# Kernel tuning notes

Measured on AMD Instinct MI355X. Metric: run time of the kernel, lower is better.

The kernel has to match this reference:

```python
import jax, jax.numpy as jnp
import numpy as np

# OAdder2d_Q, mode='oconv', in_bit=16, w_bit=16 (dorefa), bias=False, no augment.
# Physical model (O2NN-style differential detection):
#   y = sum_{c,i,j} [ x*w*sin(phi)*(d0+d1)/2 + (x^2 + w^2)*(d0-d1)/4 ]
# With ideal disks (d0=d1=1) the square terms vanish and the op reduces to a
# conv whose effective kernel is w * sin(phi); default oconv phases are -pi/2
# for the first C//2 input channels and +pi/2 for the rest.

IN_BIT = 16
W_BIT = 16
STRIDE = 1
PADDING = 1
B, C, O, K, H, W = 32, 128, 256, 3, 56, 56


def _ste_round(v, n):
    # straight-through round (forward value == torch uniform_quantize)
    return v + jax.lax.stop_gradient(jnp.round(v * n) / n - v)


def input_quantize(x):
    n = float(2 ** IN_BIT - 1)
    return _ste_round(jnp.clip(x, 0.0, 1.0), n)


def weight_quantize(w):
    # dorefa, w_bit > 1
    n = float(2 ** W_BIT - 1)
    t = jnp.tanh(w)
    t = t / (2.0 * jnp.max(jnp.abs(t))) + 0.5
    return _ste_round(t, n)


def _conv(x, k):
    return jax.lax.conv_general_dilated(
        x, k, (STRIDE, STRIDE), [(PADDING, PADDING), (PADDING, PADDING)],
        dimension_numbers=("NCHW", "OIHW", "NCHW"))


def optical_conv2d(x_q, w_q, phases, disks):
    s = jnp.sin(phases)[0, 0]                  # (C,k,k)
    d0 = disks[0, 0, ..., 0]                   # (C,k,k)
    d1 = disks[0, 0, ..., 1]
    k_mul = w_q * (s * (d0 + d1) * 0.5)        # effective conv kernel (O,C,k,k)
    y = _conv(x_q, k_mul)                      # (N,O,H,W)
    coef = (d0 - d1) * 0.25                    # zero for ideal disks
    y_sq = _conv(x_q * x_q, coef[None])        # (N,1,H,W), broadcasts over O
    w_term = jnp.sum(w_q * w_q * coef[None], axis=(1, 2, 3))  # (O,)
    return y + y_sq + w_term[None, :, None, None]


def setup_inputs() -> dict:
    key = jax.random.key(0)
    k1, k2 = jax.random.split(key)
    x = jax.random.uniform(k1, (B, C, H, W), dtype=jnp.float32)
    fan_in = C * K * K
    weight = jax.random.normal(k2, (O, C, K, K), dtype=jnp.float32) * np.sqrt(2.0 / fan_in)
    phases = jnp.concatenate([
        jnp.full((1, 1, C // 2, K, K), -np.pi / 2, dtype=jnp.float32),
        jnp.full((1, 1, C - C // 2, K, K), np.pi / 2, dtype=jnp.float32)], axis=2)
    disks = jnp.ones((1, 1, C, K, K, 2), dtype=jnp.float32)
    return {"x": x, "weight": weight, "phases": phases, "disks": disks}


def reference(x, weight, phases, disks):
    x_q = input_quantize(x)
    w_q = weight_quantize(weight)
    return optical_conv2d(x_q, w_q, phases, disks)
```

## Files before the change

### kernel.cpp

```cpp
#include <hip/hip_runtime.h>
#include <math.h>

typedef __attribute__((ext_vector_type(8))) short short8;
typedef __attribute__((ext_vector_type(4))) float floatx4;

#define BB 32
#define CC 128
#define OO 256
#define HH 56
#define WW 56
#define HWSZ 3136
#define NPIX 100352
#define WELEM 294912
#define QN 65535.0f
#define QINV (1.0f/65535.0f)

#define MAXB_OFF   0
#define CFLAG_OFF  128
#define WTERM_OFF  256
#define COEF_OFF   2048
#define KEFF_OFF   8192
#define YSQ_OFF    598016
#define XQP_OFF    1048576
#define XQP_BYTES  30408704ull
#define WS_NEED    (XQP_OFF + XQP_BYTES)
#define KEFF32_OFF 8192

__device__ __forceinline__ float quant_x(float v) {
    v = fminf(fmaxf(v, 0.0f), 1.0f);
    return rintf(v * QN) * QINV;
}

__device__ __forceinline__ unsigned short f2bf(float f) {
    unsigned u = __float_as_uint(f);
    u += 0x7fffu + ((u >> 16) & 1u);
    return (unsigned short)(u >> 16);
}

__device__ __forceinline__ void gl16(const void* g, void* l) {
    __builtin_amdgcn_global_load_lds(
        (const __attribute__((address_space(1))) unsigned char*)g,
        (__attribute__((address_space(3))) unsigned char*)l, 16, 0, 0);
}

__global__ void kmax_kernel(const float* __restrict__ w, unsigned* __restrict__ maxout) {
    int i = blockIdx.x * blockDim.x + threadIdx.x;
    float m = 0.0f;
    for (int idx = i; idx < WELEM; idx += gridDim.x * blockDim.x)
        m = fmaxf(m, fabsf(w[idx]));
    #pragma unroll
    for (int off = 32; off; off >>= 1)
        m = fmaxf(m, __shfl_down(m, off));
    __shared__ float red[4];
    if ((threadIdx.x & 63) == 0) red[threadIdx.x >> 6] = m;
    __syncthreads();
    if (threadIdx.x == 0) {
        m = fmaxf(fmaxf(red[0], red[1]), fmaxf(red[2], red[3]));
        atomicMax(maxout, __float_as_uint(m));
    }
}

__global__ void kprep_kernel(const float* __restrict__ wt, const float* __restrict__ phases,
                             const float* __restrict__ disks, const unsigned* __restrict__ maxbits,
                             unsigned short* __restrict__ kefft, float* __restrict__ coef,
                             unsigned* __restrict__ cflag, float* __restrict__ wterm) {
    int idx = blockIdx.x * blockDim.x + threadIdx.x;
    if (idx >= WELEM) return;
    int kk = idx % 9;
    int c  = (idx / 9) % CC;
    int o  = idx / (9 * CC);
    float M = tanhf(__uint_as_float(*maxbits));
    float t = tanhf(wt[idx]);
    float v = t / (2.0f * M) + 0.5f;
    float wq = rintf(v * QN) * QINV;
    int pidx = c * 9 + kk;
    float s  = sinf(phases[pidx]);
    float d0 = disks[pidx * 2 + 0];
    float d1 = disks[pidx * 2 + 1];
    float kv = wq * (s * (d0 + d1) * 0.5f);

    int step = kk * 4 + (c >> 5);
    int ot = o >> 7, lo = o & 127;
    int wm = lo >> 6, mf = (lo >> 4) & 3, l15 = lo & 15;
    int kg = (c >> 3) & 3, e = c & 7;
    size_t byte = (size_t)(step * 2 + ot) * 8192
                + wm * 4096 + mf * 1024 + (kg * 16 + l15) * 16 + e * 2;
    kefft[byte >> 1] = f2bf(kv);

    float cf = (d0 - d1) * 0.25f;
    if (o == 0) {
        coef[kk * CC + c] = cf;
        if (cf != 0.0f) atomicOr(cflag, 1u);
    }
    float contrib = wq * wq * cf;
    if (contrib != 0.0f) atomicAdd(wterm + o, contrib);
}

__global__ __launch_bounds__(256) void kborder_kernel(unsigned short* __restrict__ xqp) {
    int t = threadIdx.x;
    int id = blockIdx.x * 256 + t;
    int b = blockIdx.y;
    int pxi = id >> 4, chunk = id & 15;
    int h, w;
    if (pxi < 128) { h = (pxi >> 6) * 57; w = pxi & 63; }
    else { int r = pxi - 128; h = 1 + (r >> 3); int wi = r & 7; w = wi == 0 ? 0 : 56 + wi; }
    short8 z = (short8)0;
    *reinterpret_cast<short8*>((char*)xqp + (size_t)b * 3801088ull
                               + ((size_t)(h * 64 + w)) * 256 + chunk * 16) = z;
}

__global__ __launch_bounds__(256) void kxqpad_kernel(const float* __restrict__ x,
                                                     unsigned short* __restrict__ xqp) {
    __shared__ __align__(16) unsigned short tile[64][136];
    int t = threadIdx.x;
    int b = blockIdx.y;
    int hw0 = blockIdx.x * 64;
    const float* xb = x + (size_t)b * (CC * HWSZ) + hw0;
    #pragma unroll
    for (int rep = 0; rep < 32; ++rep) {
        int lin = rep * 256 + t;
        int c = lin >> 6, j = lin & 63;
        float v = xb[(size_t)c * HWSZ + j];
        tile[j][c] = f2bf(quant_x(v));
    }
    __syncthreads();
    unsigned short* xq_b = xqp + (size_t)b * (58 * 64 * 128);
    #pragma unroll
    for (int rep = 0; rep < 4; ++rep) {
        int lin = rep * 256 + t;
        int c16 = lin & 15, j = lin >> 4;
        int hw = hw0 + j;
        int h = hw / WW, w = hw - h * WW;
        short8 v = *reinterpret_cast<const short8*>(&tile[j][c16 * 8]);
        *reinterpret_cast<short8*>(xq_b + ((size_t)((h + 1) * 64 + (w + 1))) * 128 + c16 * 8) = v;
    }
}

__global__ __launch_bounds__(256) void ysq_kernel(const float* __restrict__ x,
                                                  const float* __restrict__ coef,
                                                  const unsigned* __restrict__ cflag,
                                                  float* __restrict__ ysq) {
    int t = threadIdx.x;
    int P = blockIdx.x * 256 + t;
    if (*cflag == 0u) {
        ysq[P] = 0.0f;
        return;
    }
    __shared__ float cf[9 * CC];
    for (int i = t; i < 9 * CC; i += 256) cf[i] = coef[i];
    __syncthreads();
    int b = P / HWSZ; int hw = P - b * HWSZ;
    int h = hw / WW;  int w = hw - h * WW;
    const float* xb = x + (size_t)b * (CC * HWSZ);
    float s2 = 0.0f;
    #pragma unroll
    for (int kk = 0; kk < 9; ++kk) {
        int dh = kk / 3 - 1, dw = kk % 3 - 1;
        int ih = h + dh, iw = w + dw;
        bool valid = ((unsigned)ih < HH) && ((unsigned)iw < WW);
        int ihc = min(max(ih, 0), HH - 1), iwc = min(max(iw, 0), WW - 1);
        const float* xp = xb + ihc * WW + iwc;
        float fm = valid ? 1.0f : 0.0f;
        const float* cp = cf + kk * CC;
        #pragma unroll 4
        for (int c = 0; c < CC; ++c) {
            float xv = quant_x(xp[(size_t)c * HWSZ]) * fm;
            s2 = fmaf(xv * xv, cp[c], s2);
        }
    }
    ysq[P] = s2;
}

__global__ __launch_bounds__(256, 2) void oconv_kernel(
        const unsigned short* __restrict__ xqp,
        const unsigned short* __restrict__ keff,
        const float* __restrict__ ysq,
        const float* __restrict__ wterm,
        float* __restrict__ out) {
    __shared__ __align__(16) char smem[32768];
    const int t  = threadIdx.x;
    const int id  = blockIdx.x;
    const int swz = (id & 7) * 196 + (id >> 3);
    const int bx  = swz >> 1;
    const int oty = swz & 1;

    const char* xb = (const char*)xqp;
    long bb0, bb1;
    {
        int pxA  = ((t >> 6) << 4) + (t & 15);
        int cOff = ((t >> 4) & 3) * 16;
        int P0 = bx * 128 + pxA;
        int b0 = P0 / HWSZ, hw0 = P0 - b0 * HWSZ;
        int h0 = hw0 / WW,  w0 = hw0 - h0 * WW;
        bb0 = ((long)((b0 * 58 + h0 + 1) * 64 + (w0 + 1))) * 256 + cOff;
        int P1 = P0 + 64;
        int b1 = P1 / HWSZ, hw1 = P1 - b1 * HWSZ;
        int h1 = hw1 / WW,  w1 = hw1 - h1 * WW;
        bb1 = ((long)((b1 * 58 + h1 + 1) * 64 + (w1 + 1))) * 256 + cOff;
    }

    const int l15 = t & 15;
    const int kg  = (t >> 4) & 3;
    const int wid = t >> 6;
    const int wm  = wid >> 1, wn = wid & 1;
    const int lane16 = (t & 63) * 16;

    floatx4 acc[4][4];
    #pragma unroll
    for (int i = 0; i < 4; ++i)
        #pragma unroll
        for (int j = 0; j < 4; ++j) acc[i][j] = (floatx4)0.0f;

    auto stage = [&](int buf, int s) {
        char* la = smem + buf * 16384 + t * 16;
        const char* ga = (const char*)keff + (size_t)(s * 2 + oty) * 8192 + t * 16;
        gl16(ga,        la);
        gl16(ga + 4096, la + 4096);
        int kk = s >> 2, cs = s & 3;
        int dh = kk / 3, dw = kk - dh * 3;
        long bo = (long)((dh - 1) * 64 + (dw - 1)) * 256 + cs * 64;
        char* lb = la + 8192;
        gl16(xb + bb0 + bo, lb);
        gl16(xb + bb1 + bo, lb + 4096);
    };

    auto compute = [&](int buf) {
        const char* base = smem + buf * 16384;
        const char* ap = base + wm * 4096 + lane16;
        const char* bp = base + 8192 + wn * 4096 + lane16;
        short8 a[4], b[4];
        #pragma unroll
        for (int mf = 0; mf < 4; ++mf)
            a[mf] = *reinterpret_cast<const short8*>(ap + mf * 1024);
        #pragma unroll
        for (int nf = 0; nf < 4; ++nf)
            b[nf] = *reinterpret_cast<const short8*>(bp + nf * 1024);
        #pragma unroll
        for (int mf = 0; mf < 4; ++mf)
            #pragma unroll
            for (int nf = 0; nf < 4; ++nf)
                acc[mf][nf] = __builtin_amdgcn_mfma_f32_16x16x32_bf16(a[mf], b[nf], acc[mf][nf], 0, 0, 0);
    };

    stage(0, 0);
    stage(1, 1);
    for (int s = 0; s < 36; ++s) {
        if (s < 35) { asm volatile("s_waitcnt vmcnt(4)" ::: "memory"); }
        else        { asm volatile("s_waitcnt vmcnt(0)" ::: "memory"); }
        __builtin_amdgcn_sched_barrier(0);
        __builtin_amdgcn_s_barrier();
        compute(s & 1);
        asm volatile("s_waitcnt lgkmcnt(0)" ::: "memory");
        __builtin_amdgcn_sched_barrier(0);
        __builtin_amdgcn_s_barrier();
        if (s < 34) stage(s & 1, s + 2);
    }

    float wv[4][4];
    #pragma unroll
    for (int mf = 0; mf < 4; ++mf)
        #pragma unroll
        for (int j = 0; j < 4; ++j)
            wv[mf][j] = wterm[oty * 128 + wm * 64 + mf * 16 + kg * 4 + j];

    #pragma unroll
    for (int nf = 0; nf < 4; ++nf) {
        int P = bx * 128 + wn * 64 + nf * 16 + l15;
        int b = P / HWSZ; int hw = P - b * HWSZ;
        float yv = ysq[P];
        float* op = out + (size_t)b * (OO * HWSZ) + hw;
        #pragma unroll
        for (int mf = 0; mf < 4; ++mf)
            #pragma unroll
            for (int j = 0; j < 4; ++j) {
                int o = oty * 128 + wm * 64 + mf * 16 + kg * 4 + j;
                op[(size_t)o * HWSZ] = acc[mf][nf][j] + yv + wv[mf][j];
            }
    }
}

__global__ void kprep32_kernel(const float* __restrict__ wt, const float* __restrict__ phases,
                               const float* __restrict__ disks, const unsigned* __restrict__ maxbits,
                               float* __restrict__ keff, float* __restrict__ coef,
                               float* __restrict__ wterm) {
    int idx = blockIdx.x * blockDim.x + threadIdx.x;
    if (idx >= WELEM) return;
    int kk = idx % 9;
    int c  = (idx / 9) % CC;
    int o  = idx / (9 * CC);
    float M = tanhf(__uint_as_float(*maxbits));
    float t = tanhf(wt[idx]);
    float v = t / (2.0f * M) + 0.5f;
    float wq = rintf(v * QN) * QINV;
    int pidx = c * 9 + kk;
    float s  = sinf(phases[pidx]);
    float d0 = disks[pidx * 2 + 0];
    float d1 = disks[pidx * 2 + 1];
    keff[(kk * CC + c) * OO + o] = wq * (s * (d0 + d1) * 0.5f);
    float cf = (d0 - d1) * 0.25f;
    if (o == 0) coef[kk * CC + c] = cf;
    float contrib = wq * wq * cf;
    if (contrib != 0.0f) atomicAdd(wterm + o, contrib);
}

__global__ __launch_bounds__(256) void kconv32_kernel(
        const float* __restrict__ xsrc, const float* __restrict__ keff,
        const float* __restrict__ coef, const float* __restrict__ wterm,
        float* __restrict__ out) {
    int t   = blockIdx.x * 256 + threadIdx.x;
    int ocb = blockIdx.y * 16;
    int b   = t / HWSZ;
    int rem = t - b * HWSZ;
    int h   = rem / WW;
    int w   = rem - h * WW;
    float acc[16];
    #pragma unroll
    for (int i = 0; i < 16; ++i) acc[i] = 0.0f;
    float s2 = 0.0f;
    const float* xb = xsrc + (size_t)b * (CC * HWSZ);
    #pragma unroll
    for (int kh = 0; kh < 3; ++kh) {
        #pragma unroll
        for (int kw = 0; kw < 3; ++kw) {
            int ih = h + kh - 1, iw = w + kw - 1;
            bool valid = ((unsigned)ih < HH) && ((unsigned)iw < WW);
            int ihc = min(max(ih, 0), HH - 1);
            int iwc = min(max(iw, 0), WW - 1);
            const float* xp   = xb + ihc * WW + iwc;
            const float* wrow = keff + (kh * 3 + kw) * (CC * OO) + ocb;
            const float* cfp  = coef + (kh * 3 + kw) * CC;
            float fm = valid ? 1.0f : 0.0f;
            #pragma unroll 4
            for (int c = 0; c < CC; ++c) {
                float xv = quant_x(xp[c * HWSZ]) * fm;
                s2 = fmaf(xv * xv, cfp[c], s2);
                #pragma unroll
                for (int i = 0; i < 16; ++i)
                    acc[i] = fmaf(xv, wrow[c * OO + i], acc[i]);
            }
        }
    }
    float* op = out + (size_t)b * (OO * HWSZ) + (size_t)ocb * HWSZ + rem;
    #pragma unroll
    for (int i = 0; i < 16; ++i)
        op[i * HWSZ] = acc[i] + s2 + wterm[ocb + i];
}

extern "C" void kernel_launch(void* const* d_in, const int* in_sizes, int n_in,
                              void* d_out, int out_size, void* d_ws, size_t ws_size,
                              hipStream_t stream) {
    const float* x      = (const float*)d_in[0];
    const float* weight = (const float*)d_in[1];
    const float* phases = (const float*)d_in[2];
    const float* disks  = (const float*)d_in[3];
    float* out = (float*)d_out;

    char* ws = (char*)d_ws;
    unsigned* maxbits = (unsigned*)(ws + MAXB_OFF);
    unsigned* cflag   = (unsigned*)(ws + CFLAG_OFF);
    float* wterm = (float*)(ws + WTERM_OFF);
    float* coef  = (float*)(ws + COEF_OFF);

    hipMemsetAsync(ws, 0, 1280, stream);
    kmax_kernel<<<288, 256, 0, stream>>>(weight, maxbits);

    if (ws_size >= WS_NEED) {
        unsigned short* kefft = (unsigned short*)(ws + KEFF_OFF);
        float* ysq = (float*)(ws + YSQ_OFF);
        unsigned short* xqp = (unsigned short*)(ws + XQP_OFF);

        kprep_kernel<<<(WELEM + 255) / 256, 256, 0, stream>>>(weight, phases, disks,
                                                              maxbits, kefft, coef, cflag, wterm);
        kborder_kernel<<<dim3(36, BB), 256, 0, stream>>>(xqp);
        kxqpad_kernel<<<dim3(49, BB), 256, 0, stream>>>(x, xqp);
        ysq_kernel<<<NPIX / 256, 256, 0, stream>>>(x, coef, cflag, ysq);
        oconv_kernel<<<1568, 256, 0, stream>>>(xqp, kefft, ysq, wterm, out);
    } else {
        float* keff32 = (float*)(ws + KEFF32_OFF);
        kprep32_kernel<<<(WELEM + 255) / 256, 256, 0, stream>>>(weight, phases, disks,
                                                                maxbits, keff32, coef, wterm);
        kconv32_kernel<<<dim3(NPIX / 256, OO / 16), 256, 0, stream>>>(x, keff32, coef, wterm, out);
    }
}
```

Baseline: 239.7 us.

## Preload full per-block weight slice into LDS and stream activations directly from global

Restructures the implicit-GEMM conv so each block owns a 32-output-channel slice and keeps its entire bf16 weight panel (all 9 taps by 128 channels, 72 KB) in dynamic LDS, loaded once up front. Activations are read directly from global/L2 into registers per tap, with no double-buffered staging or per-step barriers. The weight layout in kprep is changed to match. The trade-off is a smaller M tile (32 vs 128), so activation traffic is repeated across 8 output blocks, and global loads sit unhidden on the MFMA critical path. LDS use is raised to 72 KB per block while the kernel requests 4 blocks per CU.

```diff
diff --git a/kernel.cpp b/kernel.cpp
--- a/kernel.cpp
+++ b/kernel.cpp
@@ -80,11 +80,11 @@
     float kv = wq * (s * (d0 + d1) * 0.5f);
 
     int step = kk * 4 + (c >> 5);
-    int ot = o >> 7, lo = o & 127;
-    int wm = lo >> 6, mf = (lo >> 4) & 3, l15 = lo & 15;
+    int ob = o >> 5, lo = o & 31;
+    int mf = (lo >> 4) & 1, l15 = lo & 15;
     int kg = (c >> 3) & 3, e = c & 7;
-    size_t byte = (size_t)(step * 2 + ot) * 8192
-                + wm * 4096 + mf * 1024 + (kg * 16 + l15) * 16 + e * 2;
+    size_t byte = (size_t)ob * 73728 + (size_t)step * 2048
+                + mf * 1024 + (kg * 16 + l15) * 16 + e * 2;
     kefft[byte >> 1] = f2bf(kv);
 
     float cf = (d0 - d1) * 0.25f;
@@ -171,110 +171,95 @@
     ysq[P] = s2;
 }
 
-__global__ __launch_bounds__(256, 2) void oconv_kernel(
+__global__ __launch_bounds__(256, 4) void oconv_kernel(
         const unsigned short* __restrict__ xqp,
         const unsigned short* __restrict__ keff,
         const float* __restrict__ ysq,
         const float* __restrict__ wterm,
         float* __restrict__ out) {
-    __shared__ __align__(16) char smem[32768];
+    extern __shared__ __align__(16) char alds[];
     const int t  = threadIdx.x;
-    const int id  = blockIdx.x;
-    const int swz = (id & 7) * 196 + (id >> 3);
-    const int bx  = swz >> 1;
-    const int oty = swz & 1;
-
-    const char* xb = (const char*)xqp;
-    long bb0, bb1;
+    const int bx = blockIdx.x;
+    const int ob = blockIdx.y;
+
     {
-        int pxA  = ((t >> 6) << 4) + (t & 15);
-        int cOff = ((t >> 4) & 3) * 16;
-        int P0 = bx * 128 + pxA;
-        int b0 = P0 / HWSZ, hw0 = P0 - b0 * HWSZ;
-        int h0 = hw0 / WW,  w0 = hw0 - h0 * WW;
-        bb0 = ((long)((b0 * 58 + h0 + 1) * 64 + (w0 + 1))) * 256 + cOff;
-        int P1 = P0 + 64;
-        int b1 = P1 / HWSZ, hw1 = P1 - b1 * HWSZ;
-        int h1 = hw1 / WW,  w1 = hw1 - h1 * WW;
-        bb1 = ((long)((b1 * 58 + h1 + 1) * 64 + (w1 + 1))) * 256 + cOff;
+        const char* ga = (const char*)keff + (size_t)ob * 73728 + t * 16;
+        char* la = alds + t * 16;
+        #pragma unroll
+        for (int i = 0; i < 18; ++i)
+            gl16(ga + i * 4096, la + i * 4096);
     }
 
     const int l15 = t & 15;
     const int kg  = (t >> 4) & 3;
-    const int wid = t >> 6;
-    const int wm  = wid >> 1, wn = wid & 1;
+    const int wv_ = t >> 6;
+
+    const char* xb = (const char*)xqp;
+    long pxb[4];
+    #pragma unroll
+    for (int nf = 0; nf < 4; ++nf) {
+        int P = bx * 256 + wv_ * 64 + nf * 16 + l15;
+        int b = P / HWSZ, hw = P - b * HWSZ;
+        int h = hw / WW,  ww = hw - h * WW;
+        pxb[nf] = ((long)((b * 58 + h + 1) * 64 + (ww + 1))) * 256 + kg * 16;
+    }
+
+    floatx4 acc[2][4];
+    #pragma unroll
+    for (int i = 0; i < 2; ++i)
+        #pragma unroll
+        for (int j = 0; j < 4; ++j) acc[i][j] = (floatx4)0.0f;
+
+    __syncthreads();
+
     const int lane16 = (t & 63) * 16;
-
-    floatx4 acc[4][4];
-    #pragma unroll
-    for (int i = 0; i < 4; ++i)
-        #pragma unroll
-        for (int j = 0; j < 4; ++j) acc[i][j] = (floatx4)0.0f;
-
-    auto stage = [&](int buf, int s) {
-        char* la = smem + buf * 16384 + t * 16;
-        const char* ga = (const char*)keff + (size_t)(s * 2 + oty) * 8192 + t * 16;
-        gl16(ga,        la);
-        gl16(ga + 4096, la + 4096);
-        int kk = s >> 2, cs = s & 3;
-        int dh = kk / 3, dw = kk - dh * 3;
-        long bo = (long)((dh - 1) * 64 + (dw - 1)) * 256 + cs * 64;
-        char* lb = la + 8192;
-        gl16(xb + bb0 + bo, lb);
-        gl16(xb + bb1 + bo, lb + 4096);
-    };
-
-    auto compute = [&](int buf) {
-        const char* base = smem + buf * 16384;
-        const char* ap = base + wm * 4096 + lane16;
-        const char* bp = base + 8192 + wn * 4096 + lane16;
-        short8 a[4], b[4];
-        #pragma unroll
-        for (int mf = 0; mf < 4; ++mf)
-            a[mf] = *reinterpret_cast<const short8*>(ap + mf * 1024);
-        #pragma unroll
-        for (int nf = 0; nf < 4; ++nf)
-            b[nf] = *reinterpret_cast<const short8*>(bp + nf * 1024);
-        #pragma unroll
-        for (int mf = 0; mf < 4; ++mf)
-            #pragma unroll
-            for (int nf = 0; nf < 4; ++nf)
-                acc[mf][nf] = __builtin_amdgcn_mfma_f32_16x16x32_bf16(a[mf], b[nf], acc[mf][nf], 0, 0, 0);
-    };
-
-    stage(0, 0);
-    stage(1, 1);
-    for (int s = 0; s < 36; ++s) {
-        if (s < 35) { asm volatile("s_waitcnt vmcnt(4)" ::: "memory"); }
-        else        { asm volatile("s_waitcnt vmcnt(0)" ::: "memory"); }
-        __builtin_amdgcn_sched_barrier(0);
-        __builtin_amdgcn_s_barrier();
-        compute(s & 1);
-        asm volatile("s_waitcnt lgkmcnt(0)" ::: "memory");
-        __builtin_amdgcn_sched_barrier(0);
-        __builtin_amdgcn_s_barrier();
-        if (s < 34) stage(s & 1, s + 2);
-    }
-
-    float wv[4][4];
-    #pragma unroll
-    for (int mf = 0; mf < 4; ++mf)
+    #pragma unroll
+    for (int kk = 0; kk < 9; ++kk) {
+        const int dh = kk / 3, dw = kk - dh * 3;
+        const long bo = (long)((dh - 1) * 64 + (dw - 1)) * 256;
+        const char* bp0 = xb + pxb[0] + bo;
+        const char* bp1 = xb + pxb[1] + bo;
+        const char* bp2 = xb + pxb[2] + bo;
+        const char* bp3 = xb + pxb[3] + bo;
+        #pragma unroll
+        for (int cs = 0; cs < 4; ++cs) {
+            const int s = kk * 4 + cs;
+            short8 b0 = *reinterpret_cast<const short8*>(bp0 + cs * 64);
+            short8 b1 = *reinterpret_cast<const short8*>(bp1 + cs * 64);
+            short8 b2 = *reinterpret_cast<const short8*>(bp2 + cs * 64);
+            short8 b3 = *reinterpret_cast<const short8*>(bp3 + cs * 64);
+            short8 a0 = *reinterpret_cast<const short8*>(alds + s * 2048 + lane16);
+            short8 a1 = *reinterpret_cast<const short8*>(alds + s * 2048 + 1024 + lane16);
+            acc[0][0] = __builtin_amdgcn_mfma_f32_16x16x32_bf16(a0, b0, acc[0][0], 0, 0, 0);
+            acc[0][1] = __builtin_amdgcn_mfma_f32_16x16x32_bf16(a0, b1, acc[0][1], 0, 0, 0);
+            acc[0][2] = __builtin_amdgcn_mfma_f32_16x16x32_bf16(a0, b2, acc[0][2], 0, 0, 0);
+            acc[0][3] = __builtin_amdgcn_mfma_f32_16x16x32_bf16(a0, b3, acc[0][3], 0, 0, 0);
+            acc[1][0] = __builtin_amdgcn_mfma_f32_16x16x32_bf16(a1, b0, acc[1][0], 0, 0, 0);
+            acc[1][1] = __builtin_amdgcn_mfma_f32_16x16x32_bf16(a1, b1, acc[1][1], 0, 0, 0);
+            acc[1][2] = __builtin_amdgcn_mfma_f32_16x16x32_bf16(a1, b2, acc[1][2], 0, 0, 0);
+            acc[1][3] = __builtin_amdgcn_mfma_f32_16x16x32_bf16(a1, b3, acc[1][3], 0, 0, 0);
+        }
+    }
+
+    float wvv[2][4];
+    #pragma unroll
+    for (int mf = 0; mf < 2; ++mf)
         #pragma unroll
         for (int j = 0; j < 4; ++j)
-            wv[mf][j] = wterm[oty * 128 + wm * 64 + mf * 16 + kg * 4 + j];
+            wvv[mf][j] = wterm[ob * 32 + mf * 16 + kg * 4 + j];
 
     #pragma unroll
     for (int nf = 0; nf < 4; ++nf) {
-        int P = bx * 128 + wn * 64 + nf * 16 + l15;
+        int P = bx * 256 + wv_ * 64 + nf * 16 + l15;
         int b = P / HWSZ; int hw = P - b * HWSZ;
         float yv = ysq[P];
         float* op = out + (size_t)b * (OO * HWSZ) + hw;
         #pragma unroll
-        for (int mf = 0; mf < 4; ++mf)
+        for (int mf = 0; mf < 2; ++mf)
             #pragma unroll
             for (int j = 0; j < 4; ++j) {
-                int o = oty * 128 + wm * 64 + mf * 16 + kg * 4 + j;
-                op[(size_t)o * HWSZ] = acc[mf][nf][j] + yv + wv[mf][j];
+                int o = ob * 32 + mf * 16 + kg * 4 + j;
+                op[(size_t)o * HWSZ] = acc[mf][nf][j] + yv + wvv[mf][j];
             }
     }
 }
@@ -369,12 +354,15 @@
         float* ysq = (float*)(ws + YSQ_OFF);
         unsigned short* xqp = (unsigned short*)(ws + XQP_OFF);
 
+        hipFuncSetAttribute((const void*)oconv_kernel,
+                            hipFuncAttributeMaxDynamicSharedMemorySize, 73728);
+
         kprep_kernel<<<(WELEM + 255) / 256, 256, 0, stream>>>(weight, phases, disks,
                                                               maxbits, kefft, coef, cflag, wterm);
         kborder_kernel<<<dim3(36, BB), 256, 0, stream>>>(xqp);
         kxqpad_kernel<<<dim3(49, BB), 256, 0, stream>>>(x, xqp);
         ysq_kernel<<<NPIX / 256, 256, 0, stream>>>(x, coef, cflag, ysq);
-        oconv_kernel<<<1568, 256, 0, stream>>>(xqp, kefft, ysq, wterm, out);
+        oconv_kernel<<<dim3(392, 8), 256, 73728, stream>>>(xqp, kefft, ysq, wterm, out);
     } else {
         float* keff32 = (float*)(ws + KEFF32_OFF);
         kprep32_kernel<<<(WELEM + 255) / 256, 256, 0, stream>>>(weight, phases, disks,
```

New measurement: 380.2 us. 58.6% more time.

## Fuse weight prep, border, input quantize and ysq into one launch

Applied to the files above, without the earlier changes.

Folds the coefficient and flag computation into the max-reduction kernel as an extra block. Merges the weight-prep, border-zeroing, input quantize/pad and ysq kernels into a single block-indexed launch, which removes three launches and the gaps between them. The input-quantize path now reads with float4 loads. When the disk coefficients are all zero, ysq blocks exit early and oconv skips reading ysq. In exchange the branches in the merged kernel are uneven in cost, and the pieces no longer have a launch boundary between them.

```diff
diff --git a/kernel.cpp b/kernel.cpp
--- a/kernel.cpp
+++ b/kernel.cpp
@@ -15,6 +15,8 @@
 #define QN 65535.0f
 #define QINV (1.0f/65535.0f)
 
+#define XQP_BSTRIDE 475136
+
 #define MAXB_OFF   0
 #define CFLAG_OFF  128
 #define WTERM_OFF  256
@@ -26,6 +28,12 @@
 #define WS_NEED    (XQP_OFF + XQP_BYTES)
 #define KEFF32_OFF 8192
 
+#define NB_PREP 1152
+#define NB_BORD 1152
+#define NB_XQ   1568
+#define NB_YSQ  392
+#define NB_TOTAL (NB_PREP + NB_BORD + NB_XQ + NB_YSQ)
+
 __device__ __forceinline__ float quant_x(float v) {
     v = fminf(fmaxf(v, 0.0f), 1.0f);
     return rintf(v * QN) * QINV;
@@ -43,10 +51,26 @@
         (__attribute__((address_space(3))) unsigned char*)l, 16, 0, 0);
 }
 
-__global__ void kmax_kernel(const float* __restrict__ w, unsigned* __restrict__ maxout) {
+__global__ void kmaxcoef_kernel(const float* __restrict__ w, const float* __restrict__ disks,
+                                unsigned* __restrict__ maxout, float* __restrict__ coef,
+                                unsigned* __restrict__ cflag) {
+    if (blockIdx.x == 288) {
+        int t = threadIdx.x;
+        unsigned any = 0;
+        for (int i = t; i < 9 * CC; i += 256) {
+            int kk = i >> 7, c = i & (CC - 1);
+            int pidx = c * 9 + kk;
+            float d0 = disks[pidx * 2 + 0], d1 = disks[pidx * 2 + 1];
+            float cf = (d0 - d1) * 0.25f;
+            coef[i] = cf;
+            if (cf != 0.0f) any = 1;
+        }
+        if (any) atomicOr(cflag, 1u);
+        return;
+    }
     int i = blockIdx.x * blockDim.x + threadIdx.x;
     float m = 0.0f;
-    for (int idx = i; idx < WELEM; idx += gridDim.x * blockDim.x)
+    for (int idx = i; idx < WELEM; idx += 288 * 256)
         m = fmaxf(m, fabsf(w[idx]));
     #pragma unroll
     for (int off = 32; off; off >>= 1)
@@ -60,115 +84,115 @@
     }
 }
 
-__global__ void kprep_kernel(const float* __restrict__ wt, const float* __restrict__ phases,
-                             const float* __restrict__ disks, const unsigned* __restrict__ maxbits,
-                             unsigned short* __restrict__ kefft, float* __restrict__ coef,
-                             unsigned* __restrict__ cflag, float* __restrict__ wterm) {
-    int idx = blockIdx.x * blockDim.x + threadIdx.x;
-    if (idx >= WELEM) return;
-    int kk = idx % 9;
-    int c  = (idx / 9) % CC;
-    int o  = idx / (9 * CC);
-    float M = tanhf(__uint_as_float(*maxbits));
-    float t = tanhf(wt[idx]);
-    float v = t / (2.0f * M) + 0.5f;
-    float wq = rintf(v * QN) * QINV;
-    int pidx = c * 9 + kk;
-    float s  = sinf(phases[pidx]);
-    float d0 = disks[pidx * 2 + 0];
-    float d1 = disks[pidx * 2 + 1];
-    float kv = wq * (s * (d0 + d1) * 0.5f);
-
-    int step = kk * 4 + (c >> 5);
-    int ot = o >> 7, lo = o & 127;
-    int wm = lo >> 6, mf = (lo >> 4) & 3, l15 = lo & 15;
-    int kg = (c >> 3) & 3, e = c & 7;
-    size_t byte = (size_t)(step * 2 + ot) * 8192
-                + wm * 4096 + mf * 1024 + (kg * 16 + l15) * 16 + e * 2;
-    kefft[byte >> 1] = f2bf(kv);
-
-    float cf = (d0 - d1) * 0.25f;
-    if (o == 0) {
-        coef[kk * CC + c] = cf;
-        if (cf != 0.0f) atomicOr(cflag, 1u);
-    }
-    float contrib = wq * wq * cf;
-    if (contrib != 0.0f) atomicAdd(wterm + o, contrib);
-}
-
-__global__ __launch_bounds__(256) void kborder_kernel(unsigned short* __restrict__ xqp) {
-    int t = threadIdx.x;
-    int id = blockIdx.x * 256 + t;
-    int b = blockIdx.y;
-    int pxi = id >> 4, chunk = id & 15;
-    int h, w;
-    if (pxi < 128) { h = (pxi >> 6) * 57; w = pxi & 63; }
-    else { int r = pxi - 128; h = 1 + (r >> 3); int wi = r & 7; w = wi == 0 ? 0 : 56 + wi; }
-    short8 z = (short8)0;
-    *reinterpret_cast<short8*>((char*)xqp + (size_t)b * 3801088ull
-                               + ((size_t)(h * 64 + w)) * 256 + chunk * 16) = z;
-}
-
-__global__ __launch_bounds__(256) void kxqpad_kernel(const float* __restrict__ x,
-                                                     unsigned short* __restrict__ xqp) {
-    __shared__ __align__(16) unsigned short tile[64][136];
-    int t = threadIdx.x;
-    int b = blockIdx.y;
-    int hw0 = blockIdx.x * 64;
-    const float* xb = x + (size_t)b * (CC * HWSZ) + hw0;
-    #pragma unroll
-    for (int rep = 0; rep < 32; ++rep) {
-        int lin = rep * 256 + t;
-        int c = lin >> 6, j = lin & 63;
-        float v = xb[(size_t)c * HWSZ + j];
-        tile[j][c] = f2bf(quant_x(v));
-    }
-    __syncthreads();
-    unsigned short* xq_b = xqp + (size_t)b * (58 * 64 * 128);
-    #pragma unroll
-    for (int rep = 0; rep < 4; ++rep) {
-        int lin = rep * 256 + t;
-        int c16 = lin & 15, j = lin >> 4;
-        int hw = hw0 + j;
-        int h = hw / WW, w = hw - h * WW;
-        short8 v = *reinterpret_cast<const short8*>(&tile[j][c16 * 8]);
-        *reinterpret_cast<short8*>(xq_b + ((size_t)((h + 1) * 64 + (w + 1))) * 128 + c16 * 8) = v;
-    }
-}
-
-__global__ __launch_bounds__(256) void ysq_kernel(const float* __restrict__ x,
-                                                  const float* __restrict__ coef,
-                                                  const unsigned* __restrict__ cflag,
-                                                  float* __restrict__ ysq) {
-    int t = threadIdx.x;
-    int P = blockIdx.x * 256 + t;
-    if (*cflag == 0u) {
-        ysq[P] = 0.0f;
+__global__ __launch_bounds__(256) void kfused_kernel(
+        const float* __restrict__ x, const float* __restrict__ wt,
+        const float* __restrict__ phases, const float* __restrict__ disks,
+        const unsigned* __restrict__ maxbits, const unsigned* __restrict__ cflag,
+        const float* __restrict__ coef,
+        unsigned short* __restrict__ kefft, float* __restrict__ wterm,
+        unsigned short* __restrict__ xqp, float* __restrict__ ysq) {
+    __shared__ __align__(16) char shmem[17408];
+    const int bid = blockIdx.x;
+    const int t   = threadIdx.x;
+
+    if (bid < NB_PREP) {
+        int idx = bid * 256 + t;
+        int kk = idx % 9;
+        int c  = (idx / 9) % CC;
+        int o  = idx / (9 * CC);
+        float M = tanhf(__uint_as_float(*maxbits));
+        float tv = tanhf(wt[idx]);
+        float v = tv / (2.0f * M) + 0.5f;
+        float wq = rintf(v * QN) * QINV;
+        int pidx = c * 9 + kk;
+        float s  = sinf(phases[pidx]);
+        float d0 = disks[pidx * 2 + 0];
+        float d1 = disks[pidx * 2 + 1];
+        float kv = wq * (s * (d0 + d1) * 0.5f);
+        int step = kk * 4 + (c >> 5);
+        int ot = o >> 7, lo = o & 127;
+        int wm = lo >> 6, mf = (lo >> 4) & 3, l15 = lo & 15;
+        int kg = (c >> 3) & 3, e = c & 7;
+        size_t byte = (size_t)(step * 2 + ot) * 8192
+                    + wm * 4096 + mf * 1024 + (kg * 16 + l15) * 16 + e * 2;
+        kefft[byte >> 1] = f2bf(kv);
+        float cf = (d0 - d1) * 0.25f;
+        float contrib = wq * wq * cf;
+        if (contrib != 0.0f) atomicAdd(wterm + o, contrib);
         return;
     }
-    __shared__ float cf[9 * CC];
-    for (int i = t; i < 9 * CC; i += 256) cf[i] = coef[i];
-    __syncthreads();
-    int b = P / HWSZ; int hw = P - b * HWSZ;
-    int h = hw / WW;  int w = hw - h * WW;
-    const float* xb = x + (size_t)b * (CC * HWSZ);
-    float s2 = 0.0f;
-    #pragma unroll
-    for (int kk = 0; kk < 9; ++kk) {
-        int dh = kk / 3 - 1, dw = kk % 3 - 1;
-        int ih = h + dh, iw = w + dw;
-        bool valid = ((unsigned)ih < HH) && ((unsigned)iw < WW);
-        int ihc = min(max(ih, 0), HH - 1), iwc = min(max(iw, 0), WW - 1);
-        const float* xp = xb + ihc * WW + iwc;
-        float fm = valid ? 1.0f : 0.0f;
-        const float* cp = cf + kk * CC;
-        #pragma unroll 4
-        for (int c = 0; c < CC; ++c) {
-            float xv = quant_x(xp[(size_t)c * HWSZ]) * fm;
-            s2 = fmaf(xv * xv, cp[c], s2);
+
+    if (bid < NB_PREP + NB_BORD) {
+        int flat = bid - NB_PREP;
+        int b   = flat / 36;
+        int id  = (flat % 36) * 256 + t;
+        int pxi = id >> 4, chunk = id & 15;
+        int h, w;
+        if (pxi < 128) { h = (pxi >> 6) * 57; w = pxi & 63; }
+        else { int r = pxi - 128; h = 1 + (r >> 3); int wi = r & 7; w = wi == 0 ? 0 : 56 + wi; }
+        short8 z = (short8)0;
+        *reinterpret_cast<short8*>((char*)xqp + (size_t)b * (XQP_BSTRIDE * 2)
+                                   + ((size_t)(h * 64 + w)) * 256 + chunk * 16) = z;
+        return;
+    }
+
+    if (bid < NB_PREP + NB_BORD + NB_XQ) {
+        int id3 = bid - (NB_PREP + NB_BORD);
+        int bx = id3 % 49, b = id3 / 49;
+        int hw0 = bx * 64;
+        unsigned short (*tile)[136] = (unsigned short (*)[136])shmem;
+        const float* xb = x + (size_t)b * (CC * HWSZ) + hw0;
+        #pragma unroll
+        for (int rep = 0; rep < 8; ++rep) {
+            int lin = rep * 256 + t;
+            int c = lin >> 4, j4 = lin & 15;
+            float4 v = *reinterpret_cast<const float4*>(xb + (size_t)c * HWSZ + j4 * 4);
+            tile[j4 * 4 + 0][c] = f2bf(quant_x(v.x));
+            tile[j4 * 4 + 1][c] = f2bf(quant_x(v.y));
+            tile[j4 * 4 + 2][c] = f2bf(quant_x(v.z));
+            tile[j4 * 4 + 3][c] = f2bf(quant_x(v.w));
         }
-    }
-    ysq[P] = s2;
+        __syncthreads();
+        unsigned short* xq_b = xqp + (size_t)b * XQP_BSTRIDE;
+        #pragma unroll
+        for (int rep = 0; rep < 4; ++rep) {
+            int lin = rep * 256 + t;
+            int c16 = lin & 15, j = lin >> 4;
+            int hw = hw0 + j;
+            int h = hw / WW, w = hw - h * WW;
+            short8 v = *reinterpret_cast<const short8*>(&tile[j][c16 * 8]);
+            *reinterpret_cast<short8*>(xq_b + ((size_t)((h + 1) * 64 + (w + 1))) * 128 + c16 * 8) = v;
+        }
+        return;
+    }
+
+    {
+        if (*cflag == 0u) return;
+        float* cf = (float*)shmem;
+        for (int i = t; i < 9 * CC; i += 256) cf[i] = coef[i];
+        __syncthreads();
+        int P = (bid - (NB_PREP + NB_BORD + NB_XQ)) * 256 + t;
+        int b = P / HWSZ; int hw = P - b * HWSZ;
+        int h = hw / WW;  int w = hw - h * WW;
+        const float* xb = x + (size_t)b * (CC * HWSZ);
+        float s2 = 0.0f;
+        #pragma unroll
+        for (int kk = 0; kk < 9; ++kk) {
+            int dh = kk / 3 - 1, dw = kk % 3 - 1;
+            int ih = h + dh, iw = w + dw;
+            bool valid = ((unsigned)ih < HH) && ((unsigned)iw < WW);
+            int ihc = min(max(ih, 0), HH - 1), iwc = min(max(iw, 0), WW - 1);
+            const float* xp = xb + ihc * WW + iwc;
+            float fm = valid ? 1.0f : 0.0f;
+            const float* cp = cf + kk * CC;
+            #pragma unroll 4
+            for (int c = 0; c < CC; ++c) {
+                float xv = quant_x(xp[(size_t)c * HWSZ]) * fm;
+                s2 = fmaf(xv * xv, cp[c], s2);
+            }
+        }
+        ysq[P] = s2;
+    }
 }
 
 __global__ __launch_bounds__(256, 2) void oconv_kernel(
@@ -176,6 +200,7 @@
         const unsigned short* __restrict__ keff,
         const float* __restrict__ ysq,
         const float* __restrict__ wterm,
+        const unsigned* __restrict__ cflag,
         float* __restrict__ out) {
     __shared__ __align__(16) char smem[32768];
     const int t  = threadIdx.x;
@@ -183,6 +208,7 @@
     const int swz = (id & 7) * 196 + (id >> 3);
     const int bx  = swz >> 1;
     const int oty = swz & 1;
+    const bool use_ysq = (*cflag != 0u);
 
     const char* xb = (const char*)xqp;
     long bb0, bb1;
@@ -267,7 +293,8 @@
     for (int nf = 0; nf < 4; ++nf) {
         int P = bx * 128 + wn * 64 + nf * 16 + l15;
         int b = P / HWSZ; int hw = P - b * HWSZ;
-        float yv = ysq[P];
+        float yv = 0.0f;
+        if (use_ysq) yv = ysq[P];
         float* op = out + (size_t)b * (OO * HWSZ) + hw;
         #pragma unroll
         for (int mf = 0; mf < 4; ++mf)
@@ -362,21 +389,19 @@
     float* coef  = (float*)(ws + COEF_OFF);
 
     hipMemsetAsync(ws, 0, 1280, stream);
-    kmax_kernel<<<288, 256, 0, stream>>>(weight, maxbits);
 
     if (ws_size >= WS_NEED) {
         unsigned short* kefft = (unsigned short*)(ws + KEFF_OFF);
         float* ysq = (float*)(ws + YSQ_OFF);
         unsigned short* xqp = (unsigned short*)(ws + XQP_OFF);
 
-        kprep_kernel<<<(WELEM + 255) / 256, 256, 0, stream>>>(weight, phases, disks,
-                                                              maxbits, kefft, coef, cflag, wterm);
-        kborder_kernel<<<dim3(36, BB), 256, 0, stream>>>(xqp);
-        kxqpad_kernel<<<dim3(49, BB), 256, 0, stream>>>(x, xqp);
-        ysq_kernel<<<NPIX / 256, 256, 0, stream>>>(x, coef, cflag, ysq);
-        oconv_kernel<<<1568, 256, 0, stream>>>(xqp, kefft, ysq, wterm, out);
+        kmaxcoef_kernel<<<289, 256, 0, stream>>>(weight, disks, maxbits, coef, cflag);
+        kfused_kernel<<<NB_TOTAL, 256, 0, stream>>>(x, weight, phases, disks, maxbits,
+                                                    cflag, coef, kefft, wterm, xqp, ysq);
+        oconv_kernel<<<1568, 256, 0, stream>>>(xqp, kefft, ysq, wterm, cflag, out);
     } else {
         float* keff32 = (float*)(ws + KEFF32_OFF);
+        kmaxcoef_kernel<<<289, 256, 0, stream>>>(weight, disks, maxbits, coef, cflag);
         kprep32_kernel<<<(WELEM + 255) / 256, 256, 0, stream>>>(weight, phases, disks,
                                                                 maxbits, keff32, coef, wterm);
         kconv32_kernel<<<dim3(NPIX / 256, OO / 16), 256, 0, stream>>>(x, keff32, coef, wterm, out);
```

Result: faster. 225.1 us (-6.1%).
